# Kernel optimization log

Measured on AMD Instinct MI355X. Metric: run time of the kernel, lower is better.

## Reference

```python
import jax, jax.numpy as jnp
import numpy as np

DIM = 2048
INTER = 1408          # moe_inter_dim per routed expert
N_EXPERTS = 32
TOPK = 6
N_GROUPS = 8
TOPK_GROUPS = 4
ROUTE_SCALE = 2.5
SHARED_INTER = 2816   # n_shared_experts(2) * moe_inter_dim
T = 8192              # tokens (batch*seq flattened)
INIT = 0.02


def setup_inputs() -> dict:
    key = jax.random.key(0)
    k = jax.random.split(key, 8)
    x = jax.random.normal(k[0], (T, DIM), jnp.float32)
    gate_w = jax.random.normal(k[1], (N_EXPERTS, DIM), jnp.float32) * INIT
    # stacked routed-expert weights (torch Linear convention: [out, in])
    w1 = jax.random.normal(k[2], (N_EXPERTS, INTER, DIM), jnp.float32) * INIT
    w2 = jax.random.normal(k[3], (N_EXPERTS, DIM, INTER), jnp.float32) * INIT
    w3 = jax.random.normal(k[4], (N_EXPERTS, INTER, DIM), jnp.float32) * INIT
    # shared experts (single fused MLP, inter = n_shared * moe_inter_dim)
    sw1 = jax.random.normal(k[5], (SHARED_INTER, DIM), jnp.float32) * INIT
    sw2 = jax.random.normal(k[6], (DIM, SHARED_INTER), jnp.float32) * INIT
    sw3 = jax.random.normal(k[7], (SHARED_INTER, DIM), jnp.float32) * INIT
    return {"x": x, "gate_w": gate_w, "w1": w1, "w2": w2, "w3": w3,
            "sw1": sw1, "sw2": sw2, "sw3": sw3}


def _gate(x, gate_w):
    # sigmoid scores, no bias (dim != 7168), group-limited top-k routing
    scores = jax.nn.sigmoid(x @ gate_w.T)                  # (T, E)
    original = scores
    sg = scores.reshape(x.shape[0], N_GROUPS, -1)          # (T, G, E/G)
    group_scores = sg.max(axis=-1)                         # (T, G)  (amax branch)
    _, gidx = jax.lax.top_k(group_scores, TOPK_GROUPS)     # (T, Gk)
    gmask = jnp.zeros((x.shape[0], N_GROUPS), bool).at[
        jnp.arange(x.shape[0])[:, None], gidx].set(True)
    masked = jnp.where(gmask[:, :, None], sg, 0.0).reshape(x.shape[0], -1)
    _, idx = jax.lax.top_k(masked, TOPK)                   # (T, K)
    w = jnp.take_along_axis(original, idx, axis=1)         # gather pre-mask scores
    w = w / w.sum(axis=-1, keepdims=True)                  # sigmoid normalization
    w = w * ROUTE_SCALE
    return w.astype(x.dtype), idx


def reference(x, gate_w, w1, w2, w3, sw1, sw2, sw3):
    weights, idx = _gate(x, gate_w)                        # (T,K), (T,K) int
    # per-token combine weight for each expert: cw[t,e] = sum_k w[t,k]*[idx==e]
    onehot = jax.nn.one_hot(idx, N_EXPERTS, dtype=weights.dtype)  # (T,K,E)
    cw = jnp.einsum('tk,tke->et', weights, onehot)         # (E, T)

    def expert_step(acc, ew):
        W1, W2, W3, cwe = ew                               # cwe: (T,)
        h = jax.nn.silu(x @ W1.T) * (x @ W3.T)             # (T, INTER)
        return acc + cwe[:, None] * (h @ W2.T), None

    y, _ = jax.lax.scan(expert_step, jnp.zeros_like(x), (w1, w2, w3, cw))
    # shared experts MLP (SwiGLU)
    z = (jax.nn.silu(x @ sw1.T) * (x @ sw3.T)) @ sw2.T
    return y + z
```

## Files before the change

kernel.cpp:

```cpp
#include <hip/hip_runtime.h>
#include <hip/hip_bf16.h>
#include <stdint.h>

typedef unsigned short u16;

#define T_TOK 8192
#define DIM 2048
#define INTER 1408
#define NEXP 32
#define TOPK 6
#define SHINTER 2816
#define SLOTS (T_TOK * TOPK)

typedef __attribute__((ext_vector_type(8))) short bf16x8;
typedef __attribute__((ext_vector_type(4))) float f32x4;

__device__ inline u16 f2bf(float f) {
  union { float f; unsigned u; } c; c.f = f;
  unsigned r = (c.u + 0x7FFFu + ((c.u >> 16) & 1u)) >> 16;
  return (u16)r;
}
__device__ inline float bf2f(u16 h) {
  union { unsigned u; float f; } c; c.u = ((unsigned)h) << 16;
  return c.f;
}

__device__ __forceinline__ void gl16(const void* g, void* l) {
  __builtin_amdgcn_global_load_lds(
      (const __attribute__((address_space(1))) void*)g,
      (__attribute__((address_space(3))) void*)l, 16, 0, 0);
}

__global__ __launch_bounds__(256)
void gate_route_k(const float* __restrict__ x, const float* __restrict__ gw,
                  int* __restrict__ tidx, float* __restrict__ tw, int* __restrict__ counts)
{
  int lane = threadIdx.x & 63, w = threadIdx.x >> 6;
  int t = blockIdx.x * 4 + w;
  __shared__ float sc[4][32];
  __shared__ float gm[4][8];
  const float* xr = x + (size_t)t * DIM + lane * 4;
  float4 xv[8];
#pragma unroll
  for (int i = 0; i < 8; i++) xv[i] = *(const float4*)(xr + i * 256);
  for (int e = 0; e < NEXP; e++) {
    const float* g = gw + (size_t)e * DIM + lane * 4;
    float acc = 0.f;
#pragma unroll
    for (int i = 0; i < 8; i++) {
      float4 gv = *(const float4*)(g + i * 256);
      acc += xv[i].x * gv.x + xv[i].y * gv.y + xv[i].z * gv.z + xv[i].w * gv.w;
    }
#pragma unroll
    for (int off = 32; off > 0; off >>= 1) acc += __shfl_down(acc, off);
    if (lane == 0) sc[w][e] = 1.f / (1.f + __expf(-acc));
  }
  if (lane == 0) {
#pragma unroll
    for (int g = 0; g < 8; g++)
      gm[w][g] = fmaxf(fmaxf(sc[w][g*4+0], sc[w][g*4+1]), fmaxf(sc[w][g*4+2], sc[w][g*4+3]));
    unsigned gsel = 0u;
    for (int it = 0; it < 4; it++) {
      float best = -1.f; int bi = 0;
      for (int g = 0; g < 8; g++)
        if (!((gsel >> g) & 1u) && gm[w][g] > best) { best = gm[w][g]; bi = g; }
      gsel |= 1u << bi;
    }
    unsigned chosen = 0u; float wsum = 0.f;
    int ids[TOPK]; float wv[TOPK];
#pragma unroll
    for (int it = 0; it < TOPK; it++) {
      float best = -1.f; int bi = 0;
      for (int e = 0; e < NEXP; e++)
        if (((gsel >> (e >> 2)) & 1u) && !((chosen >> e) & 1u) && sc[w][e] > best) { best = sc[w][e]; bi = e; }
      chosen |= 1u << bi; ids[it] = bi; wv[it] = best; wsum += best;
    }
    float s = 2.5f / wsum;
#pragma unroll
    for (int k = 0; k < TOPK; k++) {
      tidx[t * TOPK + k] = ids[k];
      tw[t * TOPK + k] = wv[k] * s;
      atomicAdd(&counts[ids[k]], 1);
    }
  }
}

__global__ void zero32(int* p) { if (threadIdx.x < NEXP) p[threadIdx.x] = 0; }

__global__ void scan_desc_k(const int* __restrict__ counts, int* __restrict__ offs,
                            int4* __restrict__ desc128, int4* __restrict__ desc256,
                            int* __restrict__ ntiles)
{
  if (threadIdx.x != 0 || blockIdx.x != 0) return;
  int off = 0, n1 = 0, n2 = 0;
  for (int e = 0; e < NEXP; e++) {
    offs[e] = off;
    int c = counts[e];
    int nt1 = (c + 127) >> 7;
    for (int i = 0; i < nt1; i++) {
      int rem = c - i * 128;
      desc128[n1++] = make_int4(e, off + i * 128, rem < 128 ? rem : 128, 0);
    }
    int nt2 = (c + 255) >> 8;
    for (int i = 0; i < nt2; i++) {
      int rem = c - i * 256;
      desc256[n2++] = make_int4(e, off + i * 256, rem < 256 ? rem : 256, 0);
    }
    off += c;
  }
  offs[NEXP] = off;
  ntiles[0] = n1;
  ntiles[1] = n2;
}

__global__ __launch_bounds__(256)
void perm_build_k(const int* __restrict__ tidx, const float* __restrict__ tw,
                  const int* __restrict__ offs, int* __restrict__ ptok,
                  float* __restrict__ pw, int* __restrict__ slotof)
{
  int e = blockIdx.x;
  int tid = threadIdx.x, lane = tid & 63, w = tid >> 6;
  __shared__ int wsum[4];
  __shared__ int cursor;
  if (tid == 0) cursor = offs[e];
  __syncthreads();
  for (int start = 0; start < SLOTS; start += 256) {
    int i = start + tid;
    int match = (tidx[i] == e) ? 1 : 0;
    unsigned long long b = __ballot(match);
    if (lane == 0) wsum[w] = __popcll(b);
    __syncthreads();
    int base = cursor;
    int waveoff = 0;
    for (int ww = 0; ww < w; ww++) waveoff += wsum[ww];
    int total = wsum[0] + wsum[1] + wsum[2] + wsum[3];
    if (match) {
      int before = __popcll(b & ((1ull << lane) - 1ull));
      int slot = base + waveoff + before;
      ptok[slot] = i / TOPK;
      pw[slot] = tw[i];
      slotof[i] = slot;
    }
    __syncthreads();
    if (tid == 0) cursor = base + total;
  }
}

__global__ __launch_bounds__(256)
void cvt_w_k(const float* __restrict__ src, u16* __restrict__ dst, int n8)
{
  int stride = gridDim.x * 256;
  for (size_t i = (size_t)blockIdx.x * 256 + threadIdx.x; i < (size_t)n8; i += stride) {
    size_t j = i * 8;
    float4 a = *(const float4*)(src + j);
    float4 b = *(const float4*)(src + j + 4);
    union { u16 h[8]; uint4 u; } p;
    p.h[0] = f2bf(a.x); p.h[1] = f2bf(a.y); p.h[2] = f2bf(a.z); p.h[3] = f2bf(a.w);
    p.h[4] = f2bf(b.x); p.h[5] = f2bf(b.y); p.h[6] = f2bf(b.z); p.h[7] = f2bf(b.w);
    *(uint4*)(dst + j) = p.u;
  }
}


template<bool SHARED>
__global__ __launch_bounds__(512, 2)
void up8_k(const u16* __restrict__ xb,
           const u16* __restrict__ B1g, const u16* __restrict__ B3g,
           const int* __restrict__ ptok,
           const int4* __restrict__ desc, const int* __restrict__ ntiles,
           u16* __restrict__ Hout)
{
  constexpr int HLD = SHARED ? SHINTER : INTER;
  constexpr int NT = DIM / 32;
  int rt0 = blockIdx.x;
  int row_tile = (rt0 & 7) * (int)(gridDim.x >> 3) + (rt0 >> 3);
  int slot_base, rows;
  const u16 *B1, *B3;
  if constexpr (SHARED) { slot_base = row_tile * 256; rows = 256; B1 = B1g; B3 = B3g; }
  else {
    if (row_tile >= ntiles[1]) return;
    int4 d = desc[row_tile];
    slot_base = d.y; rows = d.z;
    size_t off = (size_t)d.x * (size_t)INTER * DIM;
    B1 = B1g + off; B3 = B3g + off;
  }
  int n0 = blockIdx.y * 128;
  int tid = threadIdx.x, lane = tid & 63, w = tid >> 6;
  int wr = w >> 2, wcn = w & 3;

  __shared__ u16 As[4][256][32];
  __shared__ u16 Bs[4][256][32];

  const u16 *pA[2], *pB[2];
#pragma unroll
  for (int s = 0; s < 2; s++) {
    int rl = w * 32 + s * 16 + (lane >> 2);
    int sc = (((lane & 3) ^ ((rl >> 1) & 3)) * 8);
    int tok;
    if constexpr (SHARED) tok = slot_base + rl;
    else tok = ptok[slot_base + (rl < rows ? rl : rows - 1)];
    pA[s] = xb + (size_t)tok * DIM + sc;
    const u16* mb = (s == 0) ? B1 : B3;
    pB[s] = mb + (size_t)(n0 + w * 16 + (lane >> 2)) * DIM + sc;
  }

  f32x4 acc[8][4];
#pragma unroll
  for (int m = 0; m < 8; m++)
#pragma unroll
    for (int n = 0; n < 4; n++) acc[m][n] = {0.f, 0.f, 0.f, 0.f};

  auto STAGE = [&](int t) {
    int b = t & 3, ko = t * 32;
    gl16(pA[0] + ko, &As[b][w * 32][0]);
    gl16(pA[1] + ko, &As[b][w * 32 + 16][0]);
    gl16(pB[0] + ko, &Bs[b][w * 32][0]);
    gl16(pB[1] + ko, &Bs[b][w * 32 + 16][0]);
  };
  STAGE(0); STAGE(1); STAGE(2);

  int ccol = (((lane >> 4) ^ ((lane >> 1) & 3)) * 8);
  for (int t = 0; t < NT; ++t) {
    if (t < NT - 2)       asm volatile("s_waitcnt vmcnt(8)" ::: "memory");
    else if (t == NT - 2) asm volatile("s_waitcnt vmcnt(4)" ::: "memory");
    else                  asm volatile("s_waitcnt vmcnt(0)" ::: "memory");
    __builtin_amdgcn_s_barrier();
    int b = t & 3;
    bf16x8 af[8], bv[4];
#pragma unroll
    for (int m = 0; m < 8; m++)
      af[m] = *(const bf16x8*)&As[b][wr * 128 + m * 16 + (lane & 15)][ccol];
#pragma unroll
    for (int n = 0; n < 4; n++)
      bv[n] = *(const bf16x8*)&Bs[b][wcn * 64 + n * 16 + (lane & 15)][ccol];
    if (t + 3 < NT) STAGE(t + 3);
    __builtin_amdgcn_s_setprio(1);
#pragma unroll
    for (int m = 0; m < 8; m++)
#pragma unroll
      for (int n = 0; n < 4; n++)
        acc[m][n] = __builtin_amdgcn_mfma_f32_16x16x32_bf16(af[m], bv[n], acc[m][n], 0, 0, 0);
    __builtin_amdgcn_s_setprio(0);
  }

#pragma unroll
  for (int m = 0; m < 8; m++) {
#pragma unroll
    for (int j = 0; j < 2; j++) {
      f32x4 c1 = acc[m][2 * j], c3 = acc[m][2 * j + 1];
      int col = n0 + (wcn * 2 + j) * 16 + (lane & 15);
#pragma unroll
      for (int r = 0; r < 4; r++) {
        int row_local = wr * 128 + m * 16 + (lane >> 4) * 4 + r;
        if (row_local < rows) {
          float v1 = c1[r], v3 = c3[r];
          Hout[(size_t)(slot_base + row_local) * HLD + col] =
              f2bf((v1 / (1.f + __expf(-v1))) * v3);
        }
      }
    }
  }
}

template<bool SHARED>
__global__ __launch_bounds__(512, 2)
void down8_k(const u16* __restrict__ Hin, const u16* __restrict__ Bg,
             const int4* __restrict__ desc, const int* __restrict__ ntiles,
             const float* __restrict__ pw,
             u16* __restrict__ slotout, float* __restrict__ yout)
{
  constexpr int KD = SHARED ? SHINTER : INTER;
  constexpr int NT = KD / 32;
  int rt0 = blockIdx.x;
  int row_tile = (rt0 & 7) * (int)(gridDim.x >> 3) + (rt0 >> 3);
  int slot_base, rows; const u16* B;
  if constexpr (SHARED) { slot_base = row_tile * 256; rows = 256; B = Bg; }
  else {
    if (row_tile >= ntiles[1]) return;
    int4 d = desc[row_tile]; slot_base = d.y; rows = d.z;
    B = Bg + (size_t)d.x * DIM * INTER;
  }
  int n0 = blockIdx.y * 256;
  int tid = threadIdx.x, lane = tid & 63, w = tid >> 6;
  int wr = w >> 2, wcn = w & 3;

  __shared__ u16 As[4][256][32];
  __shared__ u16 Bs[4][256][32];

  const u16 *pA[2], *pB[2];
#pragma unroll
  for (int s = 0; s < 2; s++) {
    int rl = w * 32 + s * 16 + (lane >> 2);
    int sc = (((lane & 3) ^ ((rl >> 1) & 3)) * 8);
    pA[s] = Hin + (size_t)(slot_base + rl) * KD + sc;
    pB[s] = B + (size_t)(n0 + rl) * KD + sc;
  }

  f32x4 acc[8][4];
#pragma unroll
  for (int m = 0; m < 8; m++)
#pragma unroll
    for (int n = 0; n < 4; n++) acc[m][n] = {0.f, 0.f, 0.f, 0.f};

  auto STAGE = [&](int t) {
    int b = t & 3, ko = t * 32;
    gl16(pA[0] + ko, &As[b][w * 32][0]);
    gl16(pA[1] + ko, &As[b][w * 32 + 16][0]);
    gl16(pB[0] + ko, &Bs[b][w * 32][0]);
    gl16(pB[1] + ko, &Bs[b][w * 32 + 16][0]);
  };
  STAGE(0); STAGE(1); STAGE(2);

  int ccol = (((lane >> 4) ^ ((lane >> 1) & 3)) * 8);
  for (int t = 0; t < NT; ++t) {
    if (t < NT - 2)       asm volatile("s_waitcnt vmcnt(8)" ::: "memory");
    else if (t == NT - 2) asm volatile("s_waitcnt vmcnt(4)" ::: "memory");
    else                  asm volatile("s_waitcnt vmcnt(0)" ::: "memory");
    __builtin_amdgcn_s_barrier();
    int b = t & 3;
    bf16x8 af[8], bv[4];
#pragma unroll
    for (int m = 0; m < 8; m++)
      af[m] = *(const bf16x8*)&As[b][wr * 128 + m * 16 + (lane & 15)][ccol];
#pragma unroll
    for (int n = 0; n < 4; n++)
      bv[n] = *(const bf16x8*)&Bs[b][wcn * 64 + n * 16 + (lane & 15)][ccol];
    if (t + 3 < NT) STAGE(t + 3);
    __builtin_amdgcn_s_setprio(1);
#pragma unroll
    for (int m = 0; m < 8; m++)
#pragma unroll
      for (int n = 0; n < 4; n++)
        acc[m][n] = __builtin_amdgcn_mfma_f32_16x16x32_bf16(af[m], bv[n], acc[m][n], 0, 0, 0);
    __builtin_amdgcn_s_setprio(0);
  }

#pragma unroll
  for (int m = 0; m < 8; m++) {
#pragma unroll
    for (int n = 0; n < 4; n++) {
      int col = n0 + (wcn * 4 + n) * 16 + (lane & 15);
#pragma unroll
      for (int r = 0; r < 4; r++) {
        int row_local = wr * 128 + m * 16 + (lane >> 4) * 4 + r;
        if (row_local < rows) {
          int slot = slot_base + row_local;
          if constexpr (SHARED) {
            yout[(size_t)slot * DIM + col] = acc[m][n][r];
          } else {
            slotout[(size_t)slot * DIM + col] = f2bf(acc[m][n][r] * pw[slot]);
          }
        }
      }
    }
  }
}

template<bool SHARED>
__global__ __launch_bounds__(256, 2)
void up_gemm_k(const u16* __restrict__ xb,
               const float* __restrict__ W1g, const float* __restrict__ W3g,
               const int* __restrict__ ptok,
               const int4* __restrict__ desc, const int* __restrict__ ntiles,
               u16* __restrict__ Hout)
{
  constexpr int HLD = SHARED ? SHINTER : INTER;
  int row_tile = blockIdx.x, col_tile = blockIdx.y;
  int slot_base, rows;
  const float *B1, *B3;
  if constexpr (SHARED) {
    slot_base = row_tile * 128; rows = 128; B1 = W1g; B3 = W3g;
  } else {
    if (row_tile >= ntiles[0]) return;
    int4 d = desc[row_tile];
    slot_base = d.y; rows = d.z;
    size_t off = (size_t)d.x * (size_t)INTER * DIM;
    B1 = W1g + off; B3 = W3g + off;
  }
  int n0 = col_tile * 128;
  int tid = threadIdx.x, lane = tid & 63;
  int wv = tid >> 6, wr = wv >> 1, wc = wv & 1;

  __shared__ u16 As[128][72];
  __shared__ u16 Bs1[128][72];
  __shared__ u16 Bs3[128][72];

  int ar = tid >> 3, ac = (tid & 7) * 8;
  const u16* asrc[4];
#pragma unroll
  for (int s = 0; s < 4; s++) {
    int r = s * 32 + ar;
    int tok;
    if constexpr (SHARED) tok = slot_base + r;
    else { int rr = r < rows ? r : rows - 1; tok = ptok[slot_base + rr]; }
    asrc[s] = xb + (size_t)tok * DIM + ac;
  }
  int br = tid >> 4, bc = (tid & 15) * 4;
  const float* b1p = B1 + (size_t)(n0 + br) * DIM + bc;
  const float* b3p = B3 + (size_t)(n0 + br) * DIM + bc;

  f32x4 acc1[4][4], acc3[4][4];
#pragma unroll
  for (int m = 0; m < 4; m++)
#pragma unroll
    for (int n = 0; n < 4; n++) { acc1[m][n] = {0.f,0.f,0.f,0.f}; acc3[m][n] = {0.f,0.f,0.f,0.f}; }

  for (int kk = 0; kk < DIM / 64; kk++) {
    __syncthreads();
#pragma unroll
    for (int s = 0; s < 4; s++) {
      uint4 v = *(const uint4*)(asrc[s] + kk * 64);
      *(uint4*)&As[s * 32 + ar][ac] = v;
    }
#pragma unroll
    for (int s = 0; s < 8; s++) {
      float4 v = *(const float4*)(b1p + (size_t)(s * 16) * DIM + kk * 64);
      union { u16 h[4]; uint2 q; } o;
      o.h[0] = f2bf(v.x); o.h[1] = f2bf(v.y); o.h[2] = f2bf(v.z); o.h[3] = f2bf(v.w);
      *(uint2*)&Bs1[s * 16 + br][bc] = o.q;
    }
#pragma unroll
    for (int s = 0; s < 8; s++) {
      float4 v = *(const float4*)(b3p + (size_t)(s * 16) * DIM + kk * 64);
      union { u16 h[4]; uint2 q; } o;
      o.h[0] = f2bf(v.x); o.h[1] = f2bf(v.y); o.h[2] = f2bf(v.z); o.h[3] = f2bf(v.w);
      *(uint2*)&Bs3[s * 16 + br][bc] = o.q;
    }
    __syncthreads();
#pragma unroll
    for (int h = 0; h < 2; h++) {
      bf16x8 af[4], b1f[4], b3f[4];
#pragma unroll
      for (int m = 0; m < 4; m++)
        af[m] = *(const bf16x8*)&As[wr * 64 + m * 16 + (lane & 15)][h * 32 + (lane >> 4) * 8];
#pragma unroll
      for (int n = 0; n < 4; n++) {
        b1f[n] = *(const bf16x8*)&Bs1[wc * 64 + n * 16 + (lane & 15)][h * 32 + (lane >> 4) * 8];
        b3f[n] = *(const bf16x8*)&Bs3[wc * 64 + n * 16 + (lane & 15)][h * 32 + (lane >> 4) * 8];
      }
#pragma unroll
      for (int m = 0; m < 4; m++)
#pragma unroll
        for (int n = 0; n < 4; n++) {
          acc1[m][n] = __builtin_amdgcn_mfma_f32_16x16x32_bf16(af[m], b1f[n], acc1[m][n], 0, 0, 0);
          acc3[m][n] = __builtin_amdgcn_mfma_f32_16x16x32_bf16(af[m], b3f[n], acc3[m][n], 0, 0, 0);
        }
    }
  }
#pragma unroll
  for (int m = 0; m < 4; m++) {
#pragma unroll
    for (int r = 0; r < 4; r++) {
      int row_local = wr * 64 + m * 16 + (lane >> 4) * 4 + r;
      if (row_local < rows) {
        size_t rowp = (size_t)(slot_base + row_local) * HLD + n0 + wc * 64 + (lane & 15);
#pragma unroll
        for (int n = 0; n < 4; n++) {
          float c1 = acc1[m][n][r], c3 = acc3[m][n][r];
          float hval = (c1 / (1.f + __expf(-c1))) * c3;
          Hout[rowp + n * 16] = f2bf(hval);
        }
      }
    }
  }
}

template<bool SHARED>
__global__ __launch_bounds__(256, 2)
void down_gemm_k(const u16* __restrict__ Hin, const float* __restrict__ Bg,
                 const int4* __restrict__ desc, const int* __restrict__ ntiles,
                 const float* __restrict__ pw,
                 u16* __restrict__ slotout, float* __restrict__ yout)
{
  constexpr int KD = SHARED ? SHINTER : INTER;
  constexpr int KSTEPS = KD / 64;
  int row_tile = blockIdx.x, col_tile = blockIdx.y;
  int slot_base, rows; const float* B;
  if constexpr (SHARED) { slot_base = row_tile * 128; rows = 128; B = Bg; }
  else {
    if (row_tile >= ntiles[0]) return;
    int4 d = desc[row_tile]; slot_base = d.y; rows = d.z;
    B = Bg + (size_t)d.x * DIM * INTER;
  }
  int n0 = col_tile * 128;
  int tid = threadIdx.x, lane = tid & 63;
  int wv = tid >> 6, wr = wv >> 1, wc = wv & 1;
  __shared__ u16 As[128][72];
  __shared__ u16 Bs[128][72];
  int ar = tid >> 3, ac = (tid & 7) * 8;
  const u16* asrc[4];
#pragma unroll
  for (int s = 0; s < 4; s++)
    asrc[s] = Hin + (size_t)(slot_base + s * 32 + ar) * KD + ac;
  int br = tid >> 4, bc = (tid & 15) * 4;
  const float* bp = B + (size_t)(n0 + br) * KD + bc;

  f32x4 acc[4][4];
#pragma unroll
  for (int m = 0; m < 4; m++)
#pragma unroll
    for (int n = 0; n < 4; n++) acc[m][n] = {0.f,0.f,0.f,0.f};

  for (int kk = 0; kk < KSTEPS; kk++) {
    __syncthreads();
#pragma unroll
    for (int s = 0; s < 4; s++) {
      uint4 v = *(const uint4*)(asrc[s] + kk * 64);
      *(uint4*)&As[s * 32 + ar][ac] = v;
    }
#pragma unroll
    for (int s = 0; s < 8; s++) {
      float4 v = *(const float4*)(bp + (size_t)(s * 16) * KD + kk * 64);
      union { u16 h[4]; uint2 q; } o;
      o.h[0] = f2bf(v.x); o.h[1] = f2bf(v.y); o.h[2] = f2bf(v.z); o.h[3] = f2bf(v.w);
      *(uint2*)&Bs[s * 16 + br][bc] = o.q;
    }
    __syncthreads();
#pragma unroll
    for (int h = 0; h < 2; h++) {
      bf16x8 af[4], bfv[4];
#pragma unroll
      for (int m = 0; m < 4; m++)
        af[m] = *(const bf16x8*)&As[wr * 64 + m * 16 + (lane & 15)][h * 32 + (lane >> 4) * 8];
#pragma unroll
      for (int n = 0; n < 4; n++)
        bfv[n] = *(const bf16x8*)&Bs[wc * 64 + n * 16 + (lane & 15)][h * 32 + (lane >> 4) * 8];
#pragma unroll
      for (int m = 0; m < 4; m++)
#pragma unroll
        for (int n = 0; n < 4; n++)
          acc[m][n] = __builtin_amdgcn_mfma_f32_16x16x32_bf16(af[m], bfv[n], acc[m][n], 0, 0, 0);
    }
  }
#pragma unroll
  for (int m = 0; m < 4; m++) {
#pragma unroll
    for (int r = 0; r < 4; r++) {
      int row_local = wr * 64 + m * 16 + (lane >> 4) * 4 + r;
      if (row_local < rows) {
        int slot = slot_base + row_local;
        size_t rp = (size_t)slot * DIM + n0 + wc * 64 + (lane & 15);
        if constexpr (SHARED) {
#pragma unroll
          for (int n = 0; n < 4; n++) yout[rp + n * 16] = acc[m][n][r];
        } else {
          float sw = pw[slot];
#pragma unroll
          for (int n = 0; n < 4; n++) slotout[rp + n * 16] = f2bf(acc[m][n][r] * sw);
        }
      }
    }
  }
}

__global__ __launch_bounds__(256)
void combine_k(float* __restrict__ y, const u16* __restrict__ slotout, const int* __restrict__ slotof)
{
  int t = blockIdx.x;
  int c = threadIdx.x * 8;
  size_t rp = (size_t)t * DIM + c;
  float4 a = *(const float4*)(y + rp);
  float4 b = *(const float4*)(y + rp + 4);
  float o[8] = {a.x, a.y, a.z, a.w, b.x, b.y, b.z, b.w};
#pragma unroll
  for (int k = 0; k < TOPK; k++) {
    int s = slotof[t * TOPK + k];
    uint4 v = *(const uint4*)(slotout + (size_t)s * DIM + c);
    o[0] += bf2f((u16)(v.x & 0xFFFFu)); o[1] += bf2f((u16)(v.x >> 16));
    o[2] += bf2f((u16)(v.y & 0xFFFFu)); o[3] += bf2f((u16)(v.y >> 16));
    o[4] += bf2f((u16)(v.z & 0xFFFFu)); o[5] += bf2f((u16)(v.z >> 16));
    o[6] += bf2f((u16)(v.w & 0xFFFFu)); o[7] += bf2f((u16)(v.w >> 16));
  }
  *(float4*)(y + rp)     = make_float4(o[0], o[1], o[2], o[3]);
  *(float4*)(y + rp + 4) = make_float4(o[4], o[5], o[6], o[7]);
}

extern "C" void kernel_launch(void* const* d_in, const int* in_sizes, int n_in,
                              void* d_out, int out_size, void* d_ws, size_t ws_size,
                              hipStream_t stream)
{
  const float* x   = (const float*)d_in[0];
  const float* gw  = (const float*)d_in[1];
  const float* w1  = (const float*)d_in[2];
  const float* w2  = (const float*)d_in[3];
  const float* w3  = (const float*)d_in[4];
  const float* sw1 = (const float*)d_in[5];
  const float* sw2 = (const float*)d_in[6];
  const float* sw3 = (const float*)d_in[7];
  float* y = (float*)d_out;
  char* ws = (char*)d_ws;

  int*   counts  = (int*)(ws + 0);
  int*   ntiles  = (int*)(ws + 256);
  int*   offs    = (int*)(ws + 512);
  int4*  desc128 = (int4*)(ws + 1024);
  int4*  desc256 = (int4*)(ws + 8192);
  int*   tidx    = (int*)(ws + 16384);
  float* tw      = (float*)(ws + 212992);
  int*   ptok    = (int*)(ws + 409600);
  float* pw      = (float*)(ws + 606208);
  int*   slotof  = (int*)(ws + 802816);
  u16*   xb      = (u16*)(ws + 1048576);
  u16*   H       = (u16*)(ws + 34603008ull);
  u16*   Hs      = (u16*)(ws + 173735936ull);
  u16*   sout    = (u16*)(ws + 219873280ull);
  u16*   w1b     = (u16*)(ws + 421199872ull);
  u16*   w3b     = (u16*)(ws + 605749248ull);
  u16*   w2b     = (u16*)(ws + 790298624ull);
  u16*   sw1b    = (u16*)(ws + 974848000ull);
  u16*   sw3b    = (u16*)(ws + 986382336ull);
  u16*   sw2b    = (u16*)(ws + 997916672ull);
  const unsigned long long NEED_FULL = 1009451008ull;

  zero32<<<1, 64, 0, stream>>>(counts);
  gate_route_k<<<2048, 256, 0, stream>>>(x, gw, tidx, tw, counts);
  cvt_w_k<<<2048, 256, 0, stream>>>(x, xb, T_TOK * DIM / 8);
  scan_desc_k<<<1, 64, 0, stream>>>(counts, offs, desc128, desc256, ntiles);
  perm_build_k<<<32, 256, 0, stream>>>(tidx, tw, offs, ptok, pw, slotof);

  if (ws_size >= NEED_FULL) {
    const int NW = NEXP * INTER * DIM / 8;
    const int NS = SHINTER * DIM / 8;
    cvt_w_k<<<4096, 256, 0, stream>>>(w1,  w1b,  NW);
    cvt_w_k<<<4096, 256, 0, stream>>>(w3,  w3b,  NW);
    cvt_w_k<<<4096, 256, 0, stream>>>(w2,  w2b,  NW);
    cvt_w_k<<<1024, 256, 0, stream>>>(sw1, sw1b, NS);
    cvt_w_k<<<1024, 256, 0, stream>>>(sw3, sw3b, NS);
    cvt_w_k<<<1024, 256, 0, stream>>>(sw2, sw2b, NS);

    up8_k<false><<<dim3(224, 11), 512, 0, stream>>>(xb, w1b, w3b, ptok, desc256, ntiles, H);
    up8_k<true ><<<dim3(32, 22), 512, 0, stream>>>(xb, sw1b, sw3b, ptok, desc256, ntiles, Hs);
    down8_k<true ><<<dim3(32, 8), 512, 0, stream>>>(Hs, sw2b, desc256, ntiles, pw, sout, y);
    down8_k<false><<<dim3(224, 8), 512, 0, stream>>>(H, w2b, desc256, ntiles, pw, sout, y);
  } else {
    up_gemm_k<false><<<dim3(416, 11), 256, 0, stream>>>(xb, w1, w3, ptok, desc128, ntiles, H);
    up_gemm_k<true ><<<dim3(64, 22), 256, 0, stream>>>(xb, sw1, sw3, ptok, desc128, ntiles, Hs);
    down_gemm_k<true ><<<dim3(64, 16), 256, 0, stream>>>(Hs, sw2, desc128, ntiles, pw, sout, y);
    down_gemm_k<false><<<dim3(416, 16), 256, 0, stream>>>(H, w2, desc128, ntiles, pw, sout, y);
  }

  combine_k<<<8192, 256, 0, stream>>>(y, sout, slotof);
}
```

Measured before the change: 2.320 ms.

## Restructure bf16 MoE GEMMs into ping-pong pipelined K=64 double-buffered schedule

Rewrites the up and down bf16 GEMM kernels to use 64-wide K tiles with two LDS buffers instead of four 32-wide ones. The main loop now splits each tile into eight barrier-separated phases that interleave LDS fragment reads, half-tile global-to-LDS loads and 16-MFMA bursts, so memory traffic overlaps compute more finely. It also changes the LDS swizzle to an 8-way XOR pattern for the wider rows. Separately, the permutation-building kernel moves to 1024-thread blocks to cut the number of loop iterations. The many barriers per tile add synchronisation cost, and the finer schedule may not pay off.

Measured after the change: 2.679 ms. 1.15x slower.

```diff
diff --git a/kernel.cpp b/kernel.cpp
--- a/kernel.cpp
+++ b/kernel.cpp
@@ -30,6 +30,13 @@
       (const __attribute__((address_space(1))) void*)g,
       (__attribute__((address_space(3))) void*)l, 16, 0, 0);
 }
+
+#define BAR() __builtin_amdgcn_s_barrier()
+#define LG0() asm volatile("s_waitcnt lgkmcnt(0)" ::: "memory")
+#define VM2() asm volatile("s_waitcnt vmcnt(2)" ::: "memory")
+#define VM0() asm volatile("s_waitcnt vmcnt(0)" ::: "memory")
+#define SP1() __builtin_amdgcn_s_setprio(1)
+#define SP0() __builtin_amdgcn_s_setprio(0)
 
 __global__ __launch_bounds__(256)
 void gate_route_k(const float* __restrict__ x, const float* __restrict__ gw,
@@ -113,18 +120,18 @@
   ntiles[1] = n2;
 }
 
-__global__ __launch_bounds__(256)
+__global__ __launch_bounds__(1024)
 void perm_build_k(const int* __restrict__ tidx, const float* __restrict__ tw,
                   const int* __restrict__ offs, int* __restrict__ ptok,
                   float* __restrict__ pw, int* __restrict__ slotof)
 {
   int e = blockIdx.x;
   int tid = threadIdx.x, lane = tid & 63, w = tid >> 6;
-  __shared__ int wsum[4];
+  __shared__ int wsum[16];
   __shared__ int cursor;
   if (tid == 0) cursor = offs[e];
   __syncthreads();
-  for (int start = 0; start < SLOTS; start += 256) {
+  for (int start = 0; start < SLOTS; start += 1024) {
     int i = start + tid;
     int match = (tidx[i] == e) ? 1 : 0;
     unsigned long long b = __ballot(match);
@@ -133,7 +140,9 @@
     int base = cursor;
     int waveoff = 0;
     for (int ww = 0; ww < w; ww++) waveoff += wsum[ww];
-    int total = wsum[0] + wsum[1] + wsum[2] + wsum[3];
+    int total = 0;
+#pragma unroll
+    for (int ww = 0; ww < 16; ww++) total += wsum[ww];
     if (match) {
       int before = __popcll(b & ((1ull << lane) - 1ull));
       int slot = base + waveoff + before;
@@ -162,20 +171,31 @@
 }
 
 
+#define LD_AF(b, mh, col) do { _Pragma("unroll") \
+  for (int m4 = 0; m4 < 4; m4++) \
+    af[m4] = *(const bf16x8*)&As[b][wr * 128 + ((mh) * 4 + m4) * 16 + l15][col]; } while (0)
+#define LD_BV(arr, b, col) do { _Pragma("unroll") \
+  for (int n = 0; n < 4; n++) \
+    arr[n] = *(const bf16x8*)&Bs[b][wcn * 64 + n * 16 + l15][col]; } while (0)
+#define MFMA16(mh, arr) do { SP1(); _Pragma("unroll") \
+  for (int m4 = 0; m4 < 4; m4++) { _Pragma("unroll") \
+    for (int n = 0; n < 4; n++) \
+      acc[(mh) * 4 + m4][n] = __builtin_amdgcn_mfma_f32_16x16x32_bf16(af[m4], arr[n], acc[(mh) * 4 + m4][n], 0, 0, 0); } \
+  SP0(); } while (0)
+
 template<bool SHARED>
 __global__ __launch_bounds__(512, 2)
-void up8_k(const u16* __restrict__ xb,
-           const u16* __restrict__ B1g, const u16* __restrict__ B3g,
-           const int* __restrict__ ptok,
-           const int4* __restrict__ desc, const int* __restrict__ ntiles,
-           u16* __restrict__ Hout)
+void up8p_k(const u16* __restrict__ xb,
+            const u16* __restrict__ B1g, const u16* __restrict__ B3g,
+            const int* __restrict__ ptok,
+            const int4* __restrict__ desc, const int* __restrict__ ntiles,
+            u16* __restrict__ Hout)
 {
   constexpr int HLD = SHARED ? SHINTER : INTER;
-  constexpr int NT = DIM / 32;
+  constexpr int NT = DIM / 64, NTI = NT / 2;
   int rt0 = blockIdx.x;
   int row_tile = (rt0 & 7) * (int)(gridDim.x >> 3) + (rt0 >> 3);
-  int slot_base, rows;
-  const u16 *B1, *B3;
+  int slot_base, rows; const u16 *B1, *B3;
   if constexpr (SHARED) { slot_base = row_tile * 256; rows = 256; B1 = B1g; B3 = B3g; }
   else {
     if (row_tile >= ntiles[1]) return;
@@ -187,73 +207,78 @@
   int n0 = blockIdx.y * 128;
   int tid = threadIdx.x, lane = tid & 63, w = tid >> 6;
   int wr = w >> 2, wcn = w & 3;
-
-  __shared__ u16 As[4][256][32];
-  __shared__ u16 Bs[4][256][32];
-
-  const u16 *pA[2], *pB[2];
-#pragma unroll
-  for (int s = 0; s < 2; s++) {
-    int rl = w * 32 + s * 16 + (lane >> 2);
-    int sc = (((lane & 3) ^ ((rl >> 1) & 3)) * 8);
+  int l15 = lane & 15, lhi = lane >> 4, lx = lane & 7;
+
+  __shared__ u16 As[2][256][64];
+  __shared__ u16 Bs[2][256][64];
+
+  const u16 *pA[4], *pB[4];
+  int selem = ((lane & 7) ^ (lane >> 3)) * 8;
+#pragma unroll
+  for (int q = 0; q < 4; q++) {
+    int half = q >> 1, sub = q & 1;
+    int rl = half * 128 + w * 16 + sub * 8 + (lane >> 3);
     int tok;
     if constexpr (SHARED) tok = slot_base + rl;
     else tok = ptok[slot_base + (rl < rows ? rl : rows - 1)];
-    pA[s] = xb + (size_t)tok * DIM + sc;
-    const u16* mb = (s == 0) ? B1 : B3;
-    pB[s] = mb + (size_t)(n0 + w * 16 + (lane >> 2)) * DIM + sc;
-  }
+    pA[q] = xb + (size_t)tok * DIM + selem;
+    int mat = (rl >> 4) & 1;
+    int srow = n0 + (rl >> 5) * 16 + (rl & 15);
+    pB[q] = (mat ? B3 : B1) + (size_t)srow * DIM + selem;
+  }
+  auto stA = [&](int t, int h) { size_t ko = (size_t)t * 64; int b = t & 1;
+    gl16(pA[h * 2 + 0] + ko, &As[b][h * 128 + w * 16][0]);
+    gl16(pA[h * 2 + 1] + ko, &As[b][h * 128 + w * 16 + 8][0]); };
+  auto stB = [&](int t, int h) { size_t ko = (size_t)t * 64; int b = t & 1;
+    gl16(pB[h * 2 + 0] + ko, &Bs[b][h * 128 + w * 16][0]);
+    gl16(pB[h * 2 + 1] + ko, &Bs[b][h * 128 + w * 16 + 8][0]); };
 
   f32x4 acc[8][4];
 #pragma unroll
   for (int m = 0; m < 8; m++)
 #pragma unroll
     for (int n = 0; n < 4; n++) acc[m][n] = {0.f, 0.f, 0.f, 0.f};
-
-  auto STAGE = [&](int t) {
-    int b = t & 3, ko = t * 32;
-    gl16(pA[0] + ko, &As[b][w * 32][0]);
-    gl16(pA[1] + ko, &As[b][w * 32 + 16][0]);
-    gl16(pB[0] + ko, &Bs[b][w * 32][0]);
-    gl16(pB[1] + ko, &Bs[b][w * 32 + 16][0]);
-  };
-  STAGE(0); STAGE(1); STAGE(2);
-
-  int ccol = (((lane >> 4) ^ ((lane >> 1) & 3)) * 8);
-  for (int t = 0; t < NT; ++t) {
-    if (t < NT - 2)       asm volatile("s_waitcnt vmcnt(8)" ::: "memory");
-    else if (t == NT - 2) asm volatile("s_waitcnt vmcnt(4)" ::: "memory");
-    else                  asm volatile("s_waitcnt vmcnt(0)" ::: "memory");
-    __builtin_amdgcn_s_barrier();
-    int b = t & 3;
-    bf16x8 af[8], bv[4];
-#pragma unroll
-    for (int m = 0; m < 8; m++)
-      af[m] = *(const bf16x8*)&As[b][wr * 128 + m * 16 + (lane & 15)][ccol];
-#pragma unroll
-    for (int n = 0; n < 4; n++)
-      bv[n] = *(const bf16x8*)&Bs[b][wcn * 64 + n * 16 + (lane & 15)][ccol];
-    if (t + 3 < NT) STAGE(t + 3);
-    __builtin_amdgcn_s_setprio(1);
-#pragma unroll
-    for (int m = 0; m < 8; m++)
-#pragma unroll
-      for (int n = 0; n < 4; n++)
-        acc[m][n] = __builtin_amdgcn_mfma_f32_16x16x32_bf16(af[m], bv[n], acc[m][n], 0, 0, 0);
-    __builtin_amdgcn_s_setprio(0);
+  bf16x8 af[4], bva[4], bvb[4];
+  int c0 = (lhi ^ lx) * 8, c1 = ((4 + lhi) ^ lx) * 8;
+
+  stB(0, 0); stB(0, 1); stA(0, 0); stA(0, 1); stB(1, 0);
+  VM2(); BAR();
+
+#pragma unroll 1
+  for (int i = 0; i < NTI - 1; i++) {
+    int t1 = 2 * i + 1, t2 = 2 * i + 2, t3 = 2 * i + 3;
+    LD_BV(bva, 0, c0); LD_AF(0, 0, c0); stB(t1, 1);        BAR(); LG0(); MFMA16(0, bva); BAR();
+    LD_AF(0, 1, c0);                    stA(t1, 0);        BAR(); LG0(); MFMA16(1, bva); BAR();
+    LD_BV(bvb, 0, c1); LD_AF(0, 0, c1); stA(t1, 1);        BAR(); LG0(); MFMA16(0, bvb); BAR();
+    LD_AF(0, 1, c1);                    stB(t2, 0); VM2(); BAR(); LG0(); MFMA16(1, bvb); BAR();
+    LD_BV(bva, 1, c0); LD_AF(1, 0, c0); stB(t2, 1);        BAR(); LG0(); MFMA16(0, bva); BAR();
+    LD_AF(1, 1, c0);                    stA(t2, 0);        BAR(); LG0(); MFMA16(1, bva); BAR();
+    LD_BV(bvb, 1, c1); LD_AF(1, 0, c1); stA(t2, 1);        BAR(); LG0(); MFMA16(0, bvb); BAR();
+    LD_AF(1, 1, c1);                    stB(t3, 0); VM2(); BAR(); LG0(); MFMA16(1, bvb); BAR();
+  }
+  {
+    int t1 = NT - 1;
+    LD_BV(bva, 0, c0); LD_AF(0, 0, c0); stB(t1, 1);        BAR(); LG0(); MFMA16(0, bva); BAR();
+    LD_AF(0, 1, c0);                    stA(t1, 0);        BAR(); LG0(); MFMA16(1, bva); BAR();
+    LD_BV(bvb, 0, c1); LD_AF(0, 0, c1); stA(t1, 1);        BAR(); LG0(); MFMA16(0, bvb); BAR();
+    LD_AF(0, 1, c1);                    VM0();             BAR(); LG0(); MFMA16(1, bvb); BAR();
+    LD_BV(bva, 1, c0); LD_AF(1, 0, c0);                    BAR(); LG0(); MFMA16(0, bva); BAR();
+    LD_AF(1, 1, c0);                                       BAR(); LG0(); MFMA16(1, bva); BAR();
+    LD_BV(bvb, 1, c1); LD_AF(1, 0, c1);                    BAR(); LG0(); MFMA16(0, bvb); BAR();
+    LD_AF(1, 1, c1);                                       BAR(); LG0(); MFMA16(1, bvb); BAR();
   }
 
 #pragma unroll
   for (int m = 0; m < 8; m++) {
 #pragma unroll
     for (int j = 0; j < 2; j++) {
-      f32x4 c1 = acc[m][2 * j], c3 = acc[m][2 * j + 1];
-      int col = n0 + (wcn * 2 + j) * 16 + (lane & 15);
+      f32x4 cc1 = acc[m][2 * j], cc3 = acc[m][2 * j + 1];
+      int col = n0 + (wcn * 2 + j) * 16 + l15;
 #pragma unroll
       for (int r = 0; r < 4; r++) {
-        int row_local = wr * 128 + m * 16 + (lane >> 4) * 4 + r;
+        int row_local = wr * 128 + m * 16 + lhi * 4 + r;
         if (row_local < rows) {
-          float v1 = c1[r], v3 = c3[r];
+          float v1 = cc1[r], v3 = cc3[r];
           Hout[(size_t)(slot_base + row_local) * HLD + col] =
               f2bf((v1 / (1.f + __expf(-v1))) * v3);
         }
@@ -264,13 +289,13 @@
 
 template<bool SHARED>
 __global__ __launch_bounds__(512, 2)
-void down8_k(const u16* __restrict__ Hin, const u16* __restrict__ Bg,
-             const int4* __restrict__ desc, const int* __restrict__ ntiles,
-             const float* __restrict__ pw,
-             u16* __restrict__ slotout, float* __restrict__ yout)
+void down8p_k(const u16* __restrict__ Hin, const u16* __restrict__ Bg,
+              const int4* __restrict__ desc, const int* __restrict__ ntiles,
+              const float* __restrict__ pw,
+              u16* __restrict__ slotout, float* __restrict__ yout)
 {
   constexpr int KD = SHARED ? SHINTER : INTER;
-  constexpr int NT = KD / 32;
+  constexpr int NT = KD / 64, NTI = NT / 2;
   int rt0 = blockIdx.x;
   int row_tile = (rt0 & 7) * (int)(gridDim.x >> 3) + (rt0 >> 3);
   int slot_base, rows; const u16* B;
@@ -283,66 +308,70 @@
   int n0 = blockIdx.y * 256;
   int tid = threadIdx.x, lane = tid & 63, w = tid >> 6;
   int wr = w >> 2, wcn = w & 3;
-
-  __shared__ u16 As[4][256][32];
-  __shared__ u16 Bs[4][256][32];
-
-  const u16 *pA[2], *pB[2];
-#pragma unroll
-  for (int s = 0; s < 2; s++) {
-    int rl = w * 32 + s * 16 + (lane >> 2);
-    int sc = (((lane & 3) ^ ((rl >> 1) & 3)) * 8);
-    pA[s] = Hin + (size_t)(slot_base + rl) * KD + sc;
-    pB[s] = B + (size_t)(n0 + rl) * KD + sc;
-  }
+  int l15 = lane & 15, lhi = lane >> 4, lx = lane & 7;
+
+  __shared__ u16 As[2][256][64];
+  __shared__ u16 Bs[2][256][64];
+
+  const u16 *pA[4], *pB[4];
+  int selem = ((lane & 7) ^ (lane >> 3)) * 8;
+#pragma unroll
+  for (int q = 0; q < 4; q++) {
+    int half = q >> 1, sub = q & 1;
+    int rl = half * 128 + w * 16 + sub * 8 + (lane >> 3);
+    pA[q] = Hin + (size_t)(slot_base + rl) * KD + selem;
+    pB[q] = B + (size_t)(n0 + rl) * KD + selem;
+  }
+  auto stA = [&](int t, int h) { size_t ko = (size_t)t * 64; int b = t & 1;
+    gl16(pA[h * 2 + 0] + ko, &As[b][h * 128 + w * 16][0]);
+    gl16(pA[h * 2 + 1] + ko, &As[b][h * 128 + w * 16 + 8][0]); };
+  auto stB = [&](int t, int h) { size_t ko = (size_t)t * 64; int b = t & 1;
+    gl16(pB[h * 2 + 0] + ko, &Bs[b][h * 128 + w * 16][0]);
+    gl16(pB[h * 2 + 1] + ko, &Bs[b][h * 128 + w * 16 + 8][0]); };
 
   f32x4 acc[8][4];
 #pragma unroll
   for (int m = 0; m < 8; m++)
 #pragma unroll
     for (int n = 0; n < 4; n++) acc[m][n] = {0.f, 0.f, 0.f, 0.f};
-
-  auto STAGE = [&](int t) {
-    int b = t & 3, ko = t * 32;
-    gl16(pA[0] + ko, &As[b][w * 32][0]);
-    gl16(pA[1] + ko, &As[b][w * 32 + 16][0]);
-    gl16(pB[0] + ko, &Bs[b][w * 32][0]);
-    gl16(pB[1] + ko, &Bs[b][w * 32 + 16][0]);
-  };
-  STAGE(0); STAGE(1); STAGE(2);
-
-  int ccol = (((lane >> 4) ^ ((lane >> 1) & 3)) * 8);
-  for (int t = 0; t < NT; ++t) {
-    if (t < NT - 2)       asm volatile("s_waitcnt vmcnt(8)" ::: "memory");
-    else if (t == NT - 2) asm volatile("s_waitcnt vmcnt(4)" ::: "memory");
-    else                  asm volatile("s_waitcnt vmcnt(0)" ::: "memory");
-    __builtin_amdgcn_s_barrier();
-    int b = t & 3;
-    bf16x8 af[8], bv[4];
-#pragma unroll
-    for (int m = 0; m < 8; m++)
-      af[m] = *(const bf16x8*)&As[b][wr * 128 + m * 16 + (lane & 15)][ccol];
-#pragma unroll
-    for (int n = 0; n < 4; n++)
-      bv[n] = *(const bf16x8*)&Bs[b][wcn * 64 + n * 16 + (lane & 15)][ccol];
-    if (t + 3 < NT) STAGE(t + 3);
-    __builtin_amdgcn_s_setprio(1);
-#pragma unroll
-    for (int m = 0; m < 8; m++)
-#pragma unroll
-      for (int n = 0; n < 4; n++)
-        acc[m][n] = __builtin_amdgcn_mfma_f32_16x16x32_bf16(af[m], bv[n], acc[m][n], 0, 0, 0);
-    __builtin_amdgcn_s_setprio(0);
+  bf16x8 af[4], bva[4], bvb[4];
+  int c0 = (lhi ^ lx) * 8, c1 = ((4 + lhi) ^ lx) * 8;
+
+  stB(0, 0); stB(0, 1); stA(0, 0); stA(0, 1); stB(1, 0);
+  VM2(); BAR();
+
+#pragma unroll 1
+  for (int i = 0; i < NTI - 1; i++) {
+    int t1 = 2 * i + 1, t2 = 2 * i + 2, t3 = 2 * i + 3;
+    LD_BV(bva, 0, c0); LD_AF(0, 0, c0); stB(t1, 1);        BAR(); LG0(); MFMA16(0, bva); BAR();
+    LD_AF(0, 1, c0);                    stA(t1, 0);        BAR(); LG0(); MFMA16(1, bva); BAR();
+    LD_BV(bvb, 0, c1); LD_AF(0, 0, c1); stA(t1, 1);        BAR(); LG0(); MFMA16(0, bvb); BAR();
+    LD_AF(0, 1, c1);                    stB(t2, 0); VM2(); BAR(); LG0(); MFMA16(1, bvb); BAR();
+    LD_BV(bva, 1, c0); LD_AF(1, 0, c0); stB(t2, 1);        BAR(); LG0(); MFMA16(0, bva); BAR();
+    LD_AF(1, 1, c0);                    stA(t2, 0);        BAR(); LG0(); MFMA16(1, bva); BAR();
+    LD_BV(bvb, 1, c1); LD_AF(1, 0, c1); stA(t2, 1);        BAR(); LG0(); MFMA16(0, bvb); BAR();
+    LD_AF(1, 1, c1);                    stB(t3, 0); VM2(); BAR(); LG0(); MFMA16(1, bvb); BAR();
+  }
+  {
+    int t1 = NT - 1;
+    LD_BV(bva, 0, c0); LD_AF(0, 0, c0); stB(t1, 1);        BAR(); LG0(); MFMA16(0, bva); BAR();
+    LD_AF(0, 1, c0);                    stA(t1, 0);        BAR(); LG0(); MFMA16(1, bva); BAR();
+    LD_BV(bvb, 0, c1); LD_AF(0, 0, c1); stA(t1, 1);        BAR(); LG0(); MFMA16(0, bvb); BAR();
+    LD_AF(0, 1, c1);                    VM0();             BAR(); LG0(); MFMA16(1, bvb); BAR();
+    LD_BV(bva, 1, c0); LD_AF(1, 0, c0);                    BAR(); LG0(); MFMA16(0, bva); BAR();
+    LD_AF(1, 1, c0);                                       BAR(); LG0(); MFMA16(1, bva); BAR();
+    LD_BV(bvb, 1, c1); LD_AF(1, 0, c1);                    BAR(); LG0(); MFMA16(0, bvb); BAR();
+    LD_AF(1, 1, c1);                                       BAR(); LG0(); MFMA16(1, bvb); BAR();
   }
 
 #pragma unroll
   for (int m = 0; m < 8; m++) {
 #pragma unroll
     for (int n = 0; n < 4; n++) {
-      int col = n0 + (wcn * 4 + n) * 16 + (lane & 15);
+      int col = n0 + (wcn * 4 + n) * 16 + l15;
 #pragma unroll
       for (int r = 0; r < 4; r++) {
-        int row_local = wr * 128 + m * 16 + (lane >> 4) * 4 + r;
+        int row_local = wr * 128 + m * 16 + lhi * 4 + r;
         if (row_local < rows) {
           int slot = slot_base + row_local;
           if constexpr (SHARED) {
@@ -616,7 +645,7 @@
   gate_route_k<<<2048, 256, 0, stream>>>(x, gw, tidx, tw, counts);
   cvt_w_k<<<2048, 256, 0, stream>>>(x, xb, T_TOK * DIM / 8);
   scan_desc_k<<<1, 64, 0, stream>>>(counts, offs, desc128, desc256, ntiles);
-  perm_build_k<<<32, 256, 0, stream>>>(tidx, tw, offs, ptok, pw, slotof);
+  perm_build_k<<<32, 1024, 0, stream>>>(tidx, tw, offs, ptok, pw, slotof);
 
   if (ws_size >= NEED_FULL) {
     const int NW = NEXP * INTER * DIM / 8;
@@ -628,10 +657,10 @@
     cvt_w_k<<<1024, 256, 0, stream>>>(sw3, sw3b, NS);
     cvt_w_k<<<1024, 256, 0, stream>>>(sw2, sw2b, NS);
 
-    up8_k<false><<<dim3(224, 11), 512, 0, stream>>>(xb, w1b, w3b, ptok, desc256, ntiles, H);
-    up8_k<true ><<<dim3(32, 22), 512, 0, stream>>>(xb, sw1b, sw3b, ptok, desc256, ntiles, Hs);
-    down8_k<true ><<<dim3(32, 8), 512, 0, stream>>>(Hs, sw2b, desc256, ntiles, pw, sout, y);
-    down8_k<false><<<dim3(224, 8), 512, 0, stream>>>(H, w2b, desc256, ntiles, pw, sout, y);
+    up8p_k<false><<<dim3(224, 11), 512, 0, stream>>>(xb, w1b, w3b, ptok, desc256, ntiles, H);
+    up8p_k<true ><<<dim3(32, 22), 512, 0, stream>>>(xb, sw1b, sw3b, ptok, desc256, ntiles, Hs);
+    down8p_k<true ><<<dim3(32, 8), 512, 0, stream>>>(Hs, sw2b, desc256, ntiles, pw, sout, y);
+    down8p_k<false><<<dim3(224, 8), 512, 0, stream>>>(H, w2b, desc256, ntiles, pw, sout, y);
   } else {
     up_gemm_k<false><<<dim3(416, 11), 256, 0, stream>>>(xb, w1, w3, ptok, desc128, ntiles, H);
     up_gemm_k<true ><<<dim3(64, 22), 256, 0, stream>>>(xb, sw1, sw3, ptok, desc128, ntiles, Hs);
```
